# Optimization experiments

Measured on AMD Instinct MI355X. Metric: run time of the kernel, lower is better.

## Reference

```python
import jax, jax.numpy as jnp
import numpy as np
from jax import lax

R = 14            # resolution (fixed by relative-position bias table)
N = R * R         # 196 tokens
DIM = 384
HEADS = 8
HD = DIM // HEADS
SCALE = HD ** -0.5
B = 128
C3 = DIM * 3


def _bias_idx():
    # identical algorithm to the torch module: discovery-order offset ids
    pts = [(i, j) for i in range(R) for j in range(R)]
    offs = {}
    idxs = []
    for p1 in pts:
        for p2 in pts:
            o = (abs(p1[0] - p2[0]), abs(p1[1] - p2[1]))
            if o not in offs:
                offs[o] = len(offs)
            idxs.append(offs[o])
    return np.asarray(idxs, dtype=np.int32).reshape(N, N), len(offs)


def setup_inputs() -> dict:
    key = jax.random.key(0)
    ks = iter(jax.random.split(key, 48))
    nrm = lambda shape, s=0.02: jax.random.normal(next(ks), shape, jnp.float32) * s
    idx, n_off = _bias_idx()  # n_off == 196 for R=14
    inp = {
        'll': jax.random.normal(next(ks), (B, DIM, R, R), jnp.float32),
        'lh': jax.random.normal(next(ks), (B, DIM, R, R), jnp.float32),
        'hl': jax.random.normal(next(ks), (B, DIM, R, R), jnp.float32),
        'hh': jax.random.normal(next(ks), (B, DIM, R, R), jnp.float32),
        # RepVGGDW (BN folded): depthwise 3x3 + depthwise 1x1 (per-channel scale)
        'dw3_w': nrm((C3, 1, 3, 3), 0.1), 'dw3_b': nrm((C3,)),
        'dw1_w': nrm((C3,), 0.1), 'dw1_b': nrm((C3,)),
        # high_fuse_pw: 3C -> C 1x1 (BN folded)
        'pw_w': nrm((DIM, C3)), 'pw_b': nrm((DIM,)),
        # HighFreqMHSA
        'hqkv_w': nrm((3 * DIM, DIM)), 'hqkv_b': nrm((3 * DIM,)),
        'hproj_w': nrm((DIM, DIM)), 'hproj_b': nrm((DIM,)),
        'hbias': nrm((HEADS, n_off), 0.1),
        # high FFN (hidden = 2*dim)
        'hm1_w': nrm((2 * DIM, DIM)), 'hm1_b': nrm((2 * DIM,)),
        'hm2_w': nrm((DIM, 2 * DIM)), 'hm2_b': nrm((DIM,)),
        # EffectiveSE
        'ese_w': nrm((DIM, DIM)), 'ese_b': nrm((DIM,)),
        # LowFreqCrossAttn
        'lq_w': nrm((DIM, DIM)), 'lq_b': nrm((DIM,)),
        'lkv_w': nrm((2 * DIM, DIM)), 'lkv_b': nrm((2 * DIM,)),
        'lproj_w': nrm((DIM, DIM)), 'lproj_b': nrm((DIM,)),
        'lbias': nrm((HEADS, n_off), 0.1),
        # low FFN
        'lm1_w': nrm((2 * DIM, DIM)), 'lm1_b': nrm((2 * DIM,)),
        'lm2_w': nrm((DIM, 2 * DIM)), 'lm2_b': nrm((DIM,)),
        'bias_idx': jnp.asarray(idx),  # int32 [N, N]
    }
    return inp


def _pw(x, w, b):
    # 1x1 conv == channel GEMM
    return jnp.einsum('oi,bihw->bohw', w, x) + b[None, :, None, None]


def _gelu(x):
    return jax.nn.gelu(x, approximate=False)


def _hsig(x):
    return jnp.clip(x / 6.0 + 0.5, 0.0, 1.0)


def _attn(q, k, v, bias):
    # q,k,v: [B,C,H,W]; bias: [heads,N,N]
    b = q.shape[0]
    qh = q.reshape(b, HEADS, HD, N).transpose(0, 1, 3, 2)  # [B,h,N,d]
    kh = k.reshape(b, HEADS, HD, N)                         # [B,h,d,N]
    vh = v.reshape(b, HEADS, HD, N).transpose(0, 1, 3, 2)  # [B,h,N,d]
    a = jnp.einsum('bhnd,bhdm->bhnm', qh, kh) * SCALE + bias[None]
    a = jax.nn.softmax(a, axis=-1)
    o = jnp.einsum('bhnm,bhmd->bhnd', a, vh)
    return o.transpose(0, 1, 3, 2).reshape(b, DIM, R, R)


def reference(ll, lh, hl, hh, dw3_w, dw3_b, dw1_w, dw1_b, pw_w, pw_b,
              hqkv_w, hqkv_b, hproj_w, hproj_b, hbias, hm1_w, hm1_b,
              hm2_w, hm2_b, ese_w, ese_b, lq_w, lq_b, lkv_w, lkv_b,
              lproj_w, lproj_b, lbias, lm1_w, lm1_b, lm2_w, lm2_b, bias_idx):
    # ---- high-frequency branch ----
    hc_in = jnp.concatenate([lh, hl, hh], axis=1)  # [B,3C,H,W]
    dw3 = lax.conv_general_dilated(hc_in, dw3_w, (1, 1), 'SAME',
                                   feature_group_count=C3,
                                   dimension_numbers=('NCHW', 'OIHW', 'NCHW'))
    dw3 = dw3 + dw3_b[None, :, None, None]
    dw1 = hc_in * dw1_w[None, :, None, None] + dw1_b[None, :, None, None]
    high_dw = _gelu(dw3 + dw1 + hc_in)  # RepVGGDW + GELU
    hc = _pw(high_dw, pw_w, pw_b)       # [B,C,H,W]

    qkv = _pw(hc, hqkv_w, hqkv_b)
    q, k, v = jnp.split(qkv, 3, axis=1)
    high_attn_out = hc + _pw(_attn(q, k, v, hbias[:, bias_idx]), hproj_w, hproj_b)
    refined_high = high_attn_out + _pw(_gelu(_pw(high_attn_out, hm1_w, hm1_b)), hm2_w, hm2_b)

    # ---- low-frequency branch ----
    se = ll * _hsig(_pw(ll.mean((2, 3), keepdims=True), ese_w, ese_b))
    lq = _pw(se, lq_w, lq_b)
    kv = _pw(refined_high, lkv_w, lkv_b)
    lk, lv = jnp.split(kv, 2, axis=1)
    ll_attn = se + _pw(_attn(lq, lk, lv, lbias[:, bias_idx]), lproj_w, lproj_b)
    output = ll_attn + _pw(_gelu(_pw(ll_attn, lm1_w, lm1_b)), lm2_w, lm2_b)
    return output
```

## Files before the change

kernel.cpp:

```cpp
#include <hip/hip_runtime.h>
#include <hip/hip_bf16.h>
#include <math.h>
#include <stdint.h>

#define TTOK 25088
#define NTOK 196

typedef __bf16 bf16x8_t __attribute__((ext_vector_type(8)));
typedef float f32x4_t __attribute__((ext_vector_type(4)));
typedef __hip_bfloat16 bf16;

__device__ __forceinline__ void async16(void* lds, const void* g) {
  __builtin_amdgcn_global_load_lds((const __attribute__((address_space(1))) unsigned int*)g,
                                   (__attribute__((address_space(3))) unsigned int*)lds, 16, 0, 0);
}

__device__ __forceinline__ float gelu_f(float x) {
  float u = x * (1.5957691216057308f + 0.07135481627f * x * x);
  return x / (1.0f + __expf(-u));
}

__device__ __forceinline__ float lo_bf(uint32_t u) { return __uint_as_float(u << 16); }
__device__ __forceinline__ float hi_bf(uint32_t u) { return __uint_as_float(u & 0xffff0000u); }

__device__ __forceinline__ bf16x8_t zero_bf16x8() {
  bf16x8_t v;
#pragma unroll
  for (int i = 0; i < 8; i++) v[i] = (__bf16)0.0f;
  return v;
}

template<int K, int EPI, int MT>
__global__ __launch_bounds__(MT * 2) void gemm_bt(
    const bf16* __restrict__ X, const bf16* __restrict__ W,
    const float* __restrict__ bias, const bf16* __restrict__ res,
    bf16* __restrict__ out, float* __restrict__ outf, int Co)
{
  __shared__ __align__(16) bf16 As[MT * 32];
  __shared__ __align__(16) bf16 Bs[128 * 32];
  constexpr int T = MT * 2;
  const int tid = threadIdx.x;
  const int lane = tid & 63;
  const int wv = tid >> 6;
  const int quad = lane >> 4, l15 = lane & 15;
  const int wm = (MT == 128) ? (wv >> 1) : 0;
  const int wn = (MT == 128) ? (wv & 1) : wv;
  const int t0 = blockIdx.x * MT;
  const int n0 = blockIdx.y * 128;

  f32x4_t acc[4][4];
#pragma unroll
  for (int i = 0; i < 4; i++)
#pragma unroll
    for (int j = 0; j < 4; j++) {
      acc[i][j][0] = 0.f; acc[i][j][1] = 0.f; acc[i][j][2] = 0.f; acc[i][j][3] = 0.f;
    }

  constexpr int KT = K / 32;
  for (int kk = 0; kk < KT; kk++) {
    if (kk) __syncthreads();
#pragma unroll
    for (int ch = tid; ch < MT * 4; ch += T) {
      int row = ch >> 2;
      int colb = (ch & 3) << 4;
      async16((char*)As + ch * 16,
              (const char*)X + ((size_t)(t0 + row) * K + kk * 32) * 2 + colb);
    }
#pragma unroll
    for (int ch = tid; ch < 512; ch += T) {
      int row = ch >> 2;
      int colb = (ch & 3) << 4;
      async16((char*)Bs + ch * 16,
              (const char*)W + ((size_t)(n0 + row) * K + kk * 32) * 2 + colb);
    }
    __syncthreads();
    bf16x8_t a[4], b[4];
#pragma unroll
    for (int mt = 0; mt < 4; mt++)
      a[mt] = *(const bf16x8_t*)(As + (wm * 64 + mt * 16 + l15) * 32 + quad * 8);
#pragma unroll
    for (int nt = 0; nt < 4; nt++)
      b[nt] = *(const bf16x8_t*)(Bs + (wn * 64 + nt * 16 + l15) * 32 + quad * 8);
#pragma unroll
    for (int mt = 0; mt < 4; mt++)
#pragma unroll
      for (int nt = 0; nt < 4; nt++)
        acc[mt][nt] = __builtin_amdgcn_mfma_f32_16x16x32_bf16(a[mt], b[nt], acc[mt][nt], 0, 0, 0);
  }

#pragma unroll
  for (int nt = 0; nt < 4; nt++) {
    int co = n0 + wn * 64 + nt * 16 + l15;
    float bv = bias[co];
#pragma unroll
    for (int mt = 0; mt < 4; mt++) {
#pragma unroll
      for (int r = 0; r < 4; r++) {
        int t = t0 + wm * 64 + mt * 16 + quad * 4 + r;
        float v = acc[mt][nt][r] + bv;
        if constexpr (EPI == 1) v = gelu_f(v);
        if constexpr (EPI >= 2) v += (float)res[(size_t)t * Co + co];
        if constexpr (EPI == 3) {
          int bb = t / NTOK, nsp = t % NTOK;
          outf[((size_t)bb * 384 + co) * NTOK + nsp] = v;
        } else {
          out[(size_t)t * Co + co] = bf16(v);
        }
      }
    }
  }
}

__global__ __launch_bounds__(256) void attn_kernel(
    const bf16* __restrict__ q, int sq,
    const bf16* __restrict__ kv, int skv, int kofs0, int vofs0,
    const float* __restrict__ bmat, bf16* __restrict__ outp)
{
  __shared__ __align__(16) bf16 Ks[196 * 48];
  __shared__ __align__(16) bf16 VT[48 * 208];
  __shared__ __align__(16) bf16 Pl[4 * 16 * 208];
  const int b = blockIdx.x >> 3, h = blockIdx.x & 7;
  const int tid = threadIdx.x;
  const int lane = tid & 63, wv = tid >> 6;
  const int quad = lane >> 4, l15 = lane & 15;
  const int qoff = h * 48, koff = kofs0 + h * 48, voff = vofs0 + h * 48;
  const float SC = 0.14433756729740643f;

  for (int j = 0; j < 5; j++) {
    int idx = j * 256 + tid;
    if (idx < 1176) {
      int o = idx * 16;
      int row = o / 96, colb = o % 96;
      async16((char*)Ks + o,
              (const char*)kv + ((size_t)(b * 196 + row) * skv + koff) * 2 + colb);
    }
  }
  for (int i = tid; i < 196 * 48; i += 256) {
    int mk = i / 48, d = i % 48;
    VT[d * 208 + mk] = kv[(size_t)(b * 196 + mk) * skv + voff + d];
  }
  for (int i = tid; i < 48 * 12; i += 256) {
    int d = i / 12, mk = 196 + (i % 12);
    VT[d * 208 + mk] = bf16(0.0f);
  }
  __syncthreads();

  bf16* Pw = Pl + wv * 16 * 208;

  for (int qt = wv; qt < 13; qt += 4) {
    int trow = qt * 16 + l15;
    int tl = trow < 196 ? trow : 195;
    const bf16* qrow = q + (size_t)(b * 196 + tl) * sq + qoff;
    bf16x8_t aq0 = *(const bf16x8_t*)(qrow + quad * 8);
    bf16x8_t aq1 = zero_bf16x8();
    if (quad < 2) aq1 = *(const bf16x8_t*)(qrow + 32 + quad * 8);

    f32x4_t S[13];
#pragma unroll
    for (int kt = 0; kt < 13; kt++) { S[kt][0] = 0.f; S[kt][1] = 0.f; S[kt][2] = 0.f; S[kt][3] = 0.f; }

#pragma unroll
    for (int kt = 0; kt < 13; kt++) {
      int kr = kt * 16 + l15;
      bf16x8_t bk0 = zero_bf16x8(), bk1 = zero_bf16x8();
      if (kr < 196) {
        const bf16* krow = Ks + kr * 48;
        bk0 = *(const bf16x8_t*)(krow + quad * 8);
        if (quad < 2) bk1 = *(const bf16x8_t*)(krow + 32 + quad * 8);
      }
      S[kt] = __builtin_amdgcn_mfma_f32_16x16x32_bf16(aq0, bk0, S[kt], 0, 0, 0);
      S[kt] = __builtin_amdgcn_mfma_f32_16x16x32_bf16(aq1, bk1, S[kt], 0, 0, 0);
    }

    float mrow[4] = {-1e30f, -1e30f, -1e30f, -1e30f};
#pragma unroll
    for (int kt = 0; kt < 13; kt++) {
      int m = kt * 16 + l15;
      int mc = m < 196 ? m : 195;
#pragma unroll
      for (int r = 0; r < 4; r++) {
        int qg = qt * 16 + quad * 4 + r;
        int qc = qg < 196 ? qg : 195;
        float s = S[kt][r] * SC + bmat[((size_t)h * 196 + qc) * 196 + mc];
        if (m >= 196) s = -1e30f;
        S[kt][r] = s;
        mrow[r] = fmaxf(mrow[r], s);
      }
    }
#pragma unroll
    for (int r = 0; r < 4; r++)
#pragma unroll
      for (int off = 1; off < 16; off <<= 1)
        mrow[r] = fmaxf(mrow[r], __shfl_xor(mrow[r], off));
    float srow[4] = {0.f, 0.f, 0.f, 0.f};
#pragma unroll
    for (int kt = 0; kt < 13; kt++)
#pragma unroll
      for (int r = 0; r < 4; r++) {
        float p = __expf(S[kt][r] - mrow[r]);
        S[kt][r] = p;
        srow[r] += p;
      }
#pragma unroll
    for (int r = 0; r < 4; r++) {
#pragma unroll
      for (int off = 1; off < 16; off <<= 1)
        srow[r] += __shfl_xor(srow[r], off);
      srow[r] = 1.0f / srow[r];
    }
#pragma unroll
    for (int kt = 0; kt < 13; kt++)
#pragma unroll
      for (int r = 0; r < 4; r++)
        Pw[(quad * 4 + r) * 208 + kt * 16 + l15] = bf16(S[kt][r] * srow[r]);

    f32x4_t O[3];
#pragma unroll
    for (int dt = 0; dt < 3; dt++) { O[dt][0] = 0.f; O[dt][1] = 0.f; O[dt][2] = 0.f; O[dt][3] = 0.f; }
#pragma unroll
    for (int ks = 0; ks < 7; ks++) {
      bool act = (ks < 6) || (quad < 2);
      bf16x8_t ap = zero_bf16x8();
      if (act) ap = *(const bf16x8_t*)(Pw + l15 * 208 + ks * 32 + quad * 8);
#pragma unroll
      for (int dt = 0; dt < 3; dt++) {
        bf16x8_t bv8 = zero_bf16x8();
        if (act) bv8 = *(const bf16x8_t*)(VT + (dt * 16 + l15) * 208 + ks * 32 + quad * 8);
        O[dt] = __builtin_amdgcn_mfma_f32_16x16x32_bf16(ap, bv8, O[dt], 0, 0, 0);
      }
    }
#pragma unroll
    for (int dt = 0; dt < 3; dt++)
#pragma unroll
      for (int r = 0; r < 4; r++) {
        int tq = qt * 16 + quad * 4 + r;
        if (tq < 196)
          outp[(size_t)(b * 196 + tq) * 384 + qoff + dt * 16 + l15] = bf16(O[dt][r]);
      }
  }
}

__global__ __launch_bounds__(256, 4) void conv_kernel(
    const float* __restrict__ lh, const float* __restrict__ hl, const float* __restrict__ hh,
    const float* __restrict__ w3, const float* __restrict__ b3,
    const float* __restrict__ w1, const float* __restrict__ b1,
    bf16* __restrict__ outp)
{
  __shared__ bf16 plane[64 * 198];
  const int tid = threadIdx.x;
  const int b = blockIdx.x / 18, chunk = blockIdx.x % 18;
  const int c0 = chunk * 64;
  const float* src = (c0 < 384) ? lh : (c0 < 768 ? hl : hh);
  const int cc0 = c0 % 384;
#pragma unroll 7
  for (int k = 0; k < 49; k++) {
    int idx = k * 256 + tid;
    int c = idx / 196, n = idx % 196;
    plane[c * 198 + n] = bf16(src[((size_t)b * 384 + cc0 + c) * 196 + n]);
  }
  __syncthreads();
  const int c = tid & 63;
  const int cg = c0 + c;
  float w9[9];
#pragma unroll
  for (int k = 0; k < 9; k++) w9[k] = w3[cg * 9 + k];
  w9[4] += w1[cg] + 1.0f;
  const float bb = b3[cg] + b1[cg];
  const int g = tid >> 6;

  for (int half = 0; half < 2; half++) {
    int r0 = half * 8 + 2 * g;
    if (r0 >= 14) break;
    float rw[4][14];
#pragma unroll
    for (int rr = 0; rr < 4; rr++) {
      int r = r0 - 1 + rr;
      if (r >= 0 && r < 14) {
        const uint32_t* prow = (const uint32_t*)(plane + (c * 198 + r * 14));
#pragma unroll
        for (int j = 0; j < 7; j++) {
          uint32_t u = prow[j];
          rw[rr][2 * j] = lo_bf(u);
          rw[rr][2 * j + 1] = hi_bf(u);
        }
      } else {
#pragma unroll
        for (int w = 0; w < 14; w++) rw[rr][w] = 0.f;
      }
    }
#pragma unroll
    for (int rr = 0; rr < 2; rr++) {
      int r = r0 + rr;
      const float* rm = rw[rr];
      const float* rc = rw[rr + 1];
      const float* rp = rw[rr + 2];
#pragma unroll
      for (int w = 0; w < 14; w++) {
        float s = bb + rm[w] * w9[1] + rc[w] * w9[4] + rp[w] * w9[7];
        if (w > 0)  s += rm[w - 1] * w9[0] + rc[w - 1] * w9[3] + rp[w - 1] * w9[6];
        if (w < 13) s += rm[w + 1] * w9[2] + rc[w + 1] * w9[5] + rp[w + 1] * w9[8];
        outp[((size_t)b * 196 + r * 14 + w) * 1152 + cg] = bf16(gelu_f(s));
      }
    }
  }
}

__global__ __launch_bounds__(256) void pool_kernel(
    const float* __restrict__ ll, float* __restrict__ pooled)
{
  const int b = blockIdx.x / 6, chunk = blockIdx.x % 6;
  const int c0 = chunk * 64;
  const int wv = threadIdx.x >> 6, lane = threadIdx.x & 63;
  for (int c = wv; c < 64; c += 4) {
    const float* p = ll + ((size_t)b * 384 + c0 + c) * 196;
    float v = p[lane] + p[64 + lane] + p[128 + lane] + (lane < 4 ? p[192 + lane] : 0.f);
#pragma unroll
    for (int off = 32; off; off >>= 1) v += __shfl_xor(v, off);
    if (lane == 0) pooled[b * 384 + c0 + c] = v * (1.0f / 196.0f);
  }
}

__global__ __launch_bounds__(256) void seapply_kernel(
    const float* __restrict__ ll, const float* __restrict__ pooled,
    const float* __restrict__ ew, const float* __restrict__ eb,
    bf16* __restrict__ se)
{
  __shared__ float pl[384];
  __shared__ float scale[64];
  __shared__ float plane[64][197];
  const int tid = threadIdx.x;
  const int b = blockIdx.x / 6, chunk = blockIdx.x % 6;
  const int c0 = chunk * 64;
  const int wv = tid >> 6, lane = tid & 63;

  for (int i = tid; i < 384; i += 256) pl[i] = pooled[b * 384 + i];
  for (int i = tid; i < 64 * 196; i += 256) {
    int c = i / 196, n = i % 196;
    plane[c][n] = ll[((size_t)b * 384 + c0 + c) * 196 + n];
  }
  __syncthreads();
  for (int cc = wv; cc < 64; cc += 4) {
    const float* wr = ew + (size_t)(c0 + cc) * 384;
    float v = 0.f;
#pragma unroll
    for (int j = 0; j < 6; j++) v += wr[j * 64 + lane] * pl[j * 64 + lane];
#pragma unroll
    for (int off = 32; off; off >>= 1) v += __shfl_xor(v, off);
    if (lane == 0) {
      float y = (v + eb[c0 + cc]) * (1.0f / 6.0f) + 0.5f;
      scale[cc] = fminf(fmaxf(y, 0.f), 1.f);
    }
  }
  __syncthreads();
  const int c = tid & 63;
  const float sc = scale[c];
  for (int n = tid >> 6; n < 196; n += 4)
    se[((size_t)b * 196 + n) * 384 + c0 + c] = bf16(plane[c][n] * sc);
}

__global__ __launch_bounds__(256) void wconvert_kernel(
    const float* p0, const float* p1, const float* p2, const float* p3, const float* p4,
    const float* p5, const float* p6, const float* p7, const float* p8, const float* p9,
    bf16* dst)
{
  int i = blockIdx.x * 256 + threadIdx.x;
  if (i >= 2801664) return;
  const int offs[11] = {0, 442368, 884736, 1032192, 1327104, 1622016,
                        1769472, 2064384, 2211840, 2506752, 2801664};
  const float* ps[10] = {p0, p1, p2, p3, p4, p5, p6, p7, p8, p9};
  int seg = 0;
#pragma unroll
  for (int k = 1; k < 10; k++) if (i >= offs[k]) seg = k;
  dst[i] = bf16(ps[seg][i - offs[seg]]);
}

__global__ __launch_bounds__(256) void biasmat_kernel(
    const float* __restrict__ hbias, const float* __restrict__ lbias,
    const int* __restrict__ idx, float* __restrict__ bh, float* __restrict__ bl)
{
  int i = blockIdx.x * 256 + threadIdx.x;
  if (i >= 307328) return;
  int h = i / 38416;
  int nm = i % 38416;
  int id = idx[nm];
  bh[i] = hbias[h * 196 + id];
  bl[i] = lbias[h * 196 + id];
}

extern "C" void kernel_launch(void* const* d_in, const int* in_sizes, int n_in,
                              void* d_out, int out_size, void* d_ws, size_t ws_size,
                              hipStream_t stream) {
  const float* ll     = (const float*)d_in[0];
  const float* lh     = (const float*)d_in[1];
  const float* hl     = (const float*)d_in[2];
  const float* hh     = (const float*)d_in[3];
  const float* dw3_w  = (const float*)d_in[4];
  const float* dw3_b  = (const float*)d_in[5];
  const float* dw1_w  = (const float*)d_in[6];
  const float* dw1_b  = (const float*)d_in[7];
  const float* pw_w   = (const float*)d_in[8];
  const float* pw_b   = (const float*)d_in[9];
  const float* hqkv_w = (const float*)d_in[10];
  const float* hqkv_b = (const float*)d_in[11];
  const float* hproj_w= (const float*)d_in[12];
  const float* hproj_b= (const float*)d_in[13];
  const float* hbias  = (const float*)d_in[14];
  const float* hm1_w  = (const float*)d_in[15];
  const float* hm1_b  = (const float*)d_in[16];
  const float* hm2_w  = (const float*)d_in[17];
  const float* hm2_b  = (const float*)d_in[18];
  const float* ese_w  = (const float*)d_in[19];
  const float* ese_b  = (const float*)d_in[20];
  const float* lq_w   = (const float*)d_in[21];
  const float* lq_b   = (const float*)d_in[22];
  const float* lkv_w  = (const float*)d_in[23];
  const float* lkv_b  = (const float*)d_in[24];
  const float* lproj_w= (const float*)d_in[25];
  const float* lproj_b= (const float*)d_in[26];
  const float* lbias  = (const float*)d_in[27];
  const float* lm1_w  = (const float*)d_in[28];
  const float* lm1_b  = (const float*)d_in[29];
  const float* lm2_w  = (const float*)d_in[30];
  const float* lm2_b  = (const float*)d_in[31];
  const int* bias_idx = (const int*)d_in[32];

  char* ws = (char*)d_ws;
  bf16*  WB = (bf16*)(ws);
  float* BH = (float*)(ws + 5603328);
  float* BL = (float*)(ws + 6832640);
  bf16*  A  = (bf16*)(ws + 8061952);
  bf16*  B1 = (bf16*)(ws + 65864704);
  bf16*  B2 = (bf16*)(ws + 85132288);
  bf16*  B3 = (bf16*)(ws + 104399872);
  bf16*  B4 = (bf16*)(ws + 123667456);
  bf16*  E  = (bf16*)(ws + 162202624);
  float* PO = (float*)(ws + 181470208);
  float* OUT = (float*)d_out;

  wconvert_kernel<<<10945, 256, 0, stream>>>(pw_w, hqkv_w, hproj_w, hm1_w, hm2_w,
                                             lq_w, lkv_w, lproj_w, lm1_w, lm2_w, WB);
  biasmat_kernel<<<1201, 256, 0, stream>>>(hbias, lbias, bias_idx, BH, BL);
  conv_kernel<<<2304, 256, 0, stream>>>(lh, hl, hh, dw3_w, dw3_b, dw1_w, dw1_b, A);
  pool_kernel<<<768, 256, 0, stream>>>(ll, PO);
  seapply_kernel<<<768, 256, 0, stream>>>(ll, PO, ese_w, ese_b, E);

  gemm_bt<1152, 0, 64><<<dim3(392, 3), 128, 0, stream>>>(A, WB + 0, pw_b, nullptr, B1, nullptr, 384);
  gemm_bt<384, 0, 128><<<dim3(196, 9), 256, 0, stream>>>(B1, WB + 442368, hqkv_b, nullptr, A, nullptr, 1152);
  attn_kernel<<<1024, 256, 0, stream>>>(A, 1152, A, 1152, 384, 768, BH, B2);
  gemm_bt<384, 2, 64><<<dim3(392, 3), 128, 0, stream>>>(B2, WB + 884736, hproj_b, B1, B3, nullptr, 384);
  gemm_bt<384, 1, 128><<<dim3(196, 6), 256, 0, stream>>>(B3, WB + 1032192, hm1_b, nullptr, B4, nullptr, 768);
  gemm_bt<768, 2, 64><<<dim3(392, 3), 128, 0, stream>>>(B4, WB + 1327104, hm2_b, B3, B1, nullptr, 384);

  gemm_bt<384, 0, 128><<<dim3(196, 6), 256, 0, stream>>>(B1, WB + 1769472, lkv_b, nullptr, B4, nullptr, 768);
  gemm_bt<384, 0, 64><<<dim3(392, 3), 128, 0, stream>>>(E, WB + 1622016, lq_b, nullptr, B2, nullptr, 384);
  attn_kernel<<<1024, 256, 0, stream>>>(B2, 384, B4, 768, 0, 384, BL, B1);
  gemm_bt<384, 2, 64><<<dim3(392, 3), 128, 0, stream>>>(B1, WB + 2064384, lproj_b, E, B3, nullptr, 384);
  gemm_bt<384, 1, 128><<<dim3(196, 6), 256, 0, stream>>>(B3, WB + 2211840, lm1_b, nullptr, A, nullptr, 768);
  gemm_bt<768, 3, 64><<<dim3(392, 3), 128, 0, stream>>>(A, WB + 2506752, lm2_b, B3, nullptr, OUT, 384);
}
```

Baseline: 779.0 us.

## Stream attention P through small LDS chunks, direct-load conv rows, merge prep kernels

The attention kernel no longer writes the full 16x208 probability tile per wave to LDS. It writes a 16x32 chunk just before each MFMA step, which shrinks LDS use and could raise occupancy. The depthwise conv kernel drops its LDS staging and bf16 round-trip and reads fp32 rows straight from global memory with a rolling three-row register window. Each thread now covers four rows instead of two per pass. The weight-conversion and bias-matrix kernels are merged into one launch, and the conv kernel loses its min-blocks launch bound, which may change register allocation. Extra LDS write/read pairs inside the MFMA loop and uncoalesced per-channel global reads in conv are the main risks.

```diff
diff --git a/kernel.cpp b/kernel.cpp
--- a/kernel.cpp
+++ b/kernel.cpp
@@ -19,9 +19,6 @@
   float u = x * (1.5957691216057308f + 0.07135481627f * x * x);
   return x / (1.0f + __expf(-u));
 }
-
-__device__ __forceinline__ float lo_bf(uint32_t u) { return __uint_as_float(u << 16); }
-__device__ __forceinline__ float hi_bf(uint32_t u) { return __uint_as_float(u & 0xffff0000u); }
 
 __device__ __forceinline__ bf16x8_t zero_bf16x8() {
   bf16x8_t v;
@@ -118,7 +115,7 @@
 {
   __shared__ __align__(16) bf16 Ks[196 * 48];
   __shared__ __align__(16) bf16 VT[48 * 208];
-  __shared__ __align__(16) bf16 Pl[4 * 16 * 208];
+  __shared__ __align__(16) bf16 Pc[4][16 * 32];
   const int b = blockIdx.x >> 3, h = blockIdx.x & 7;
   const int tid = threadIdx.x;
   const int lane = tid & 63, wv = tid >> 6;
@@ -145,8 +142,6 @@
   }
   __syncthreads();
 
-  bf16* Pw = Pl + wv * 16 * 208;
-
   for (int qt = wv; qt < 13; qt += 4) {
     int trow = qt * 16 + l15;
     int tl = trow < 196 ? trow : 195;
@@ -208,24 +203,27 @@
         srow[r] += __shfl_xor(srow[r], off);
       srow[r] = 1.0f / srow[r];
     }
-#pragma unroll
-    for (int kt = 0; kt < 13; kt++)
-#pragma unroll
-      for (int r = 0; r < 4; r++)
-        Pw[(quad * 4 + r) * 208 + kt * 16 + l15] = bf16(S[kt][r] * srow[r]);
 
     f32x4_t O[3];
 #pragma unroll
     for (int dt = 0; dt < 3; dt++) { O[dt][0] = 0.f; O[dt][1] = 0.f; O[dt][2] = 0.f; O[dt][3] = 0.f; }
 #pragma unroll
     for (int ks = 0; ks < 7; ks++) {
-      bool act = (ks < 6) || (quad < 2);
-      bf16x8_t ap = zero_bf16x8();
-      if (act) ap = *(const bf16x8_t*)(Pw + l15 * 208 + ks * 32 + quad * 8);
+#pragma unroll
+      for (int half = 0; half < 2; half++) {
+        int kt = ks * 2 + half;
+#pragma unroll
+        for (int r = 0; r < 4; r++) {
+          float pv = (kt < 13) ? S[kt][r] * srow[r] : 0.f;
+          Pc[wv][(quad * 4 + r) * 32 + half * 16 + l15] = bf16(pv);
+        }
+      }
+      bf16x8_t ap = *(const bf16x8_t*)(&Pc[wv][l15 * 32 + quad * 8]);
 #pragma unroll
       for (int dt = 0; dt < 3; dt++) {
         bf16x8_t bv8 = zero_bf16x8();
-        if (act) bv8 = *(const bf16x8_t*)(VT + (dt * 16 + l15) * 208 + ks * 32 + quad * 8);
+        if (ks < 6 || quad < 2)
+          bv8 = *(const bf16x8_t*)(VT + (dt * 16 + l15) * 208 + ks * 32 + quad * 8);
         O[dt] = __builtin_amdgcn_mfma_f32_16x16x32_bf16(ap, bv8, O[dt], 0, 0, 0);
       }
     }
@@ -240,66 +238,59 @@
   }
 }
 
-__global__ __launch_bounds__(256, 4) void conv_kernel(
+__device__ __forceinline__ void load_row14(float* d, const float* rowp, bool valid) {
+  if (valid) {
+    const float2* p2 = (const float2*)rowp;
+#pragma unroll
+    for (int j = 0; j < 7; j++) { float2 v = p2[j]; d[2 * j] = v.x; d[2 * j + 1] = v.y; }
+  } else {
+#pragma unroll
+    for (int w = 0; w < 14; w++) d[w] = 0.f;
+  }
+}
+
+__global__ __launch_bounds__(256) void conv_kernel(
     const float* __restrict__ lh, const float* __restrict__ hl, const float* __restrict__ hh,
     const float* __restrict__ w3, const float* __restrict__ b3,
     const float* __restrict__ w1, const float* __restrict__ b1,
     bf16* __restrict__ outp)
 {
-  __shared__ bf16 plane[64 * 198];
   const int tid = threadIdx.x;
   const int b = blockIdx.x / 18, chunk = blockIdx.x % 18;
   const int c0 = chunk * 64;
   const float* src = (c0 < 384) ? lh : (c0 < 768 ? hl : hh);
   const int cc0 = c0 % 384;
-#pragma unroll 7
-  for (int k = 0; k < 49; k++) {
-    int idx = k * 256 + tid;
-    int c = idx / 196, n = idx % 196;
-    plane[c * 198 + n] = bf16(src[((size_t)b * 384 + cc0 + c) * 196 + n]);
-  }
-  __syncthreads();
   const int c = tid & 63;
+  const int g = tid >> 6;
   const int cg = c0 + c;
+  const float* base = src + ((size_t)b * 384 + cc0 + c) * 196;
+
   float w9[9];
 #pragma unroll
   for (int k = 0; k < 9; k++) w9[k] = w3[cg * 9 + k];
   w9[4] += w1[cg] + 1.0f;
   const float bb = b3[cg] + b1[cg];
-  const int g = tid >> 6;
-
-  for (int half = 0; half < 2; half++) {
-    int r0 = half * 8 + 2 * g;
-    if (r0 >= 14) break;
-    float rw[4][14];
-#pragma unroll
-    for (int rr = 0; rr < 4; rr++) {
-      int r = r0 - 1 + rr;
-      if (r >= 0 && r < 14) {
-        const uint32_t* prow = (const uint32_t*)(plane + (c * 198 + r * 14));
-#pragma unroll
-        for (int j = 0; j < 7; j++) {
-          uint32_t u = prow[j];
-          rw[rr][2 * j] = lo_bf(u);
-          rw[rr][2 * j + 1] = hi_bf(u);
-        }
-      } else {
-#pragma unroll
-        for (int w = 0; w < 14; w++) rw[rr][w] = 0.f;
-      }
-    }
-#pragma unroll
-    for (int rr = 0; rr < 2; rr++) {
-      int r = r0 + rr;
-      const float* rm = rw[rr];
-      const float* rc = rw[rr + 1];
-      const float* rp = rw[rr + 2];
+
+  const int r0 = 4 * g;
+  float rows[3][14];
+  load_row14(rows[0], base + (r0 - 1) * 14, r0 - 1 >= 0);
+  load_row14(rows[1], base + r0 * 14, true);
+
+#pragma unroll
+  for (int s = 0; s < 4; s++) {
+    int r = r0 + s;
+    if (r < 14) {
+      float* rp = rows[(s + 2) % 3];
+      load_row14(rp, base + (r + 1) * 14, r + 1 < 14);
+      const float* rm = rows[s % 3];
+      const float* rc = rows[(s + 1) % 3];
+      bf16* orow = outp + ((size_t)b * 196 + r * 14) * 1152 + cg;
 #pragma unroll
       for (int w = 0; w < 14; w++) {
-        float s = bb + rm[w] * w9[1] + rc[w] * w9[4] + rp[w] * w9[7];
-        if (w > 0)  s += rm[w - 1] * w9[0] + rc[w - 1] * w9[3] + rp[w - 1] * w9[6];
-        if (w < 13) s += rm[w + 1] * w9[2] + rc[w + 1] * w9[5] + rp[w + 1] * w9[8];
-        outp[((size_t)b * 196 + r * 14 + w) * 1152 + cg] = bf16(gelu_f(s));
+        float ss = bb + rm[w] * w9[1] + rc[w] * w9[4] + rp[w] * w9[7];
+        if (w > 0)  ss += rm[w - 1] * w9[0] + rc[w - 1] * w9[3] + rp[w - 1] * w9[6];
+        if (w < 13) ss += rm[w + 1] * w9[2] + rc[w + 1] * w9[5] + rp[w + 1] * w9[8];
+        orow[(size_t)w * 1152] = bf16(gelu_f(ss));
       }
     }
   }
@@ -358,33 +349,32 @@
     se[((size_t)b * 196 + n) * 384 + c0 + c] = bf16(plane[c][n] * sc);
 }
 
-__global__ __launch_bounds__(256) void wconvert_kernel(
+__global__ __launch_bounds__(256) void prep_kernel(
     const float* p0, const float* p1, const float* p2, const float* p3, const float* p4,
     const float* p5, const float* p6, const float* p7, const float* p8, const float* p9,
-    bf16* dst)
-{
-  int i = blockIdx.x * 256 + threadIdx.x;
-  if (i >= 2801664) return;
-  const int offs[11] = {0, 442368, 884736, 1032192, 1327104, 1622016,
-                        1769472, 2064384, 2211840, 2506752, 2801664};
-  const float* ps[10] = {p0, p1, p2, p3, p4, p5, p6, p7, p8, p9};
-  int seg = 0;
-#pragma unroll
-  for (int k = 1; k < 10; k++) if (i >= offs[k]) seg = k;
-  dst[i] = bf16(ps[seg][i - offs[seg]]);
-}
-
-__global__ __launch_bounds__(256) void biasmat_kernel(
+    bf16* dst,
     const float* __restrict__ hbias, const float* __restrict__ lbias,
     const int* __restrict__ idx, float* __restrict__ bh, float* __restrict__ bl)
 {
-  int i = blockIdx.x * 256 + threadIdx.x;
-  if (i >= 307328) return;
-  int h = i / 38416;
-  int nm = i % 38416;
-  int id = idx[nm];
-  bh[i] = hbias[h * 196 + id];
-  bl[i] = lbias[h * 196 + id];
+  const int bid = blockIdx.x;
+  if (bid < 10944) {
+    int i = bid * 256 + threadIdx.x;
+    const int offs[11] = {0, 442368, 884736, 1032192, 1327104, 1622016,
+                          1769472, 2064384, 2211840, 2506752, 2801664};
+    const float* ps[10] = {p0, p1, p2, p3, p4, p5, p6, p7, p8, p9};
+    int seg = 0;
+#pragma unroll
+    for (int k = 1; k < 10; k++) if (i >= offs[k]) seg = k;
+    dst[i] = bf16(ps[seg][i - offs[seg]]);
+  } else {
+    int i = (bid - 10944) * 256 + threadIdx.x;
+    if (i >= 307328) return;
+    int h = i / 38416;
+    int nm = i % 38416;
+    int id = idx[nm];
+    bh[i] = hbias[h * 196 + id];
+    bl[i] = lbias[h * 196 + id];
+  }
 }
 
 extern "C" void kernel_launch(void* const* d_in, const int* in_sizes, int n_in,
@@ -437,9 +427,9 @@
   float* PO = (float*)(ws + 181470208);
   float* OUT = (float*)d_out;
 
-  wconvert_kernel<<<10945, 256, 0, stream>>>(pw_w, hqkv_w, hproj_w, hm1_w, hm2_w,
-                                             lq_w, lkv_w, lproj_w, lm1_w, lm2_w, WB);
-  biasmat_kernel<<<1201, 256, 0, stream>>>(hbias, lbias, bias_idx, BH, BL);
+  prep_kernel<<<12145, 256, 0, stream>>>(pw_w, hqkv_w, hproj_w, hm1_w, hm2_w,
+                                         lq_w, lkv_w, lproj_w, lm1_w, lm2_w, WB,
+                                         hbias, lbias, bias_idx, BH, BL);
   conv_kernel<<<2304, 256, 0, stream>>>(lh, hl, hh, dw3_w, dw3_b, dw1_w, dw1_b, A);
   pool_kernel<<<768, 256, 0, stream>>>(ll, PO);
   seapply_kernel<<<768, 256, 0, stream>>>(ll, PO, ese_w, ese_b, E);
```

Result: slower. 857.5 us (+10.1%).
